# Performance work log

Hardware: AMD Instinct MI355X
Metric: run time of the kernel (lower is better)

The kernel has to match this reference:

```python
import jax, jax.numpy as jnp
import numpy as np

L, H, D, T, DFF, OUT, B = 6, 12, 49, 16, 1024, 10, 8192
STD = 0.02


def setup_inputs() -> dict:
    key = jax.random.key(0)
    ks = jax.random.split(key, 24)
    n = lambda k, shape: jax.random.normal(k, shape, dtype=jnp.float32) * STD
    return {
        "x": jax.random.normal(ks[0], (B, 784), dtype=jnp.float32),
        "mask": jnp.ones((B, T), dtype=bool),  # unused by the original Attention
        # per-layer, per-head Q/K/V/out linears (weights stored as (in, out))
        "Wq": n(ks[1], (L, H, D, D)), "bq": n(ks[2], (L, H, D)),
        "Wk": n(ks[3], (L, H, D, D)), "bk": n(ks[4], (L, H, D)),
        "Wv": n(ks[5], (L, H, D, D)), "bv": n(ks[6], (L, H, D)),
        "Wo": n(ks[7], (L, H, D, D)), "bo": n(ks[8], (L, H, D)),
        # concat projection Linear(D*H, D)
        "Wcat": n(ks[9], (L, H * D, D)), "bcat": n(ks[10], (L, D)),
        # LayerNorms
        "ln1_g": jnp.ones((L, D), jnp.float32), "ln1_b": jnp.zeros((L, D), jnp.float32),
        "ln2_g": jnp.ones((L, D), jnp.float32), "ln2_b": jnp.zeros((L, D), jnp.float32),
        # FeedForward
        "W1": n(ks[11], (L, D, DFF)), "b1": n(ks[12], (L, DFF)),
        "W2": n(ks[13], (L, DFF, D)), "b2": n(ks[14], (L, D)),
        # ClassificationHead
        "Wc": n(ks[15], (D, OUT)), "bc": n(ks[16], (OUT,)),
    }


def _ln(x, g, b):
    mu = jnp.mean(x, axis=-1, keepdims=True)
    var = jnp.mean((x - mu) ** 2, axis=-1, keepdims=True)
    return (x - mu) / jnp.sqrt(var + 1e-5) * g + b


def _forward(x, Wq, bq, Wk, bk, Wv, bv, Wo, bo, Wcat, bcat,
             ln1_g, ln1_b, ln2_g, ln2_b, W1, b1, W2, b2, Wc, bc):
    bsz = x.shape[0]
    h = x.reshape(bsz, T, D)  # MakeTokens
    scale = float(1.0 / np.sqrt(D))
    for i in range(L):
        xn = _ln(h, ln1_g[i], ln1_b[i])
        # all heads batched via einsum (each head attends over full d_model)
        q = jnp.einsum('btd,hde->bhte', xn, Wq[i]) + bq[i][None, :, None, :]
        k = jnp.einsum('btd,hde->bhte', xn, Wk[i]) + bk[i][None, :, None, :]
        v = jnp.einsum('btd,hde->bhte', xn, Wv[i]) + bv[i][None, :, None, :]
        w = jax.nn.softmax(jnp.einsum('bhte,bhse->bhts', q, k) * scale, axis=-1)
        o = jnp.einsum('bhts,bhse->bhte', w, v)
        o = jnp.einsum('bhte,hef->bhtf', o, Wo[i]) + bo[i][None, :, None, :]
        cat = o.transpose(0, 2, 1, 3).reshape(bsz, T, H * D)  # concat heads
        attn = cat @ Wcat[i] + bcat[i]
        x2 = h + attn  # dropout is identity at inference
        xn2 = _ln(x2, ln2_g[i], ln2_b[i])
        ff = jax.nn.relu(xn2 @ W1[i] + b1[i]) @ W2[i] + b2[i]
        h = x2 + ff
    return h[:, 0, :] @ Wc + bc  # ClassificationHead on token 0


def reference(x, mask, Wq, bq, Wk, bk, Wv, bv, Wo, bo, Wcat, bcat,
              ln1_g, ln1_b, ln2_g, ln2_b, W1, b1, W2, b2, Wc, bc):
    # mask is accepted but unused, matching the original Attention.forward
    return _forward(x, Wq, bq, Wk, bk, Wv, bv, Wo, bo, Wcat, bcat,
                    ln1_g, ln1_b, ln2_g, ln2_b, W1, b1, W2, b2, Wc, bc)
```

## Files before the change

kernel.cpp:

```cpp
#include <hip/hip_runtime.h>
#include <hip/hip_bf16.h>

#define LYR 6
#define NH 12
#define DM 49
#define FFD 1024
#define NOUT 10
#define NB 8192
#define NWIN 168
#define SPW 2

typedef __bf16 bf16x8 __attribute__((ext_vector_type(8)));
typedef float f32x4 __attribute__((ext_vector_type(4)));
typedef unsigned int u32;
typedef u32 u32x4 __attribute__((ext_vector_type(4)));

static __device__ __forceinline__ f32x4 mfma_full(u32x4 a, u32x4 b, f32x4 c) {
  return __builtin_amdgcn_mfma_f32_16x16x32_bf16(
      __builtin_bit_cast(bf16x8, a), __builtin_bit_cast(bf16x8, b), c, 0, 0, 0);
}

static __device__ __forceinline__ f32x4 mfma_hz(u32 a0, u32 a1, u32 b0, u32 b1, f32x4 c) {
  u32x4 A = {a0, a1, 0u, 0u};
  u32x4 B = {b0, b1, 0u, 0u};
  return mfma_full(A, B, c);
}

static __device__ __forceinline__ unsigned short f2bf(float f) {
  union { float f; unsigned u; } c; c.f = f;
  unsigned r = c.u + 0x7fffu + ((c.u >> 16) & 1u);
  return (unsigned short)(r >> 16);
}

static __device__ __forceinline__ u32 pk2(float a, float b) {
  __hip_bfloat162 h2 = __float22bfloat162_rn(make_float2(a, b));
  u32 r;
  __builtin_memcpy(&r, &h2, 4);
  return r;
}

static __device__ __forceinline__ void gload16(const void* gp, void* lp) {
  __builtin_amdgcn_global_load_lds(
      (const __attribute__((address_space(1))) unsigned int*)gp,
      (__attribute__((address_space(3))) unsigned int*)lp, 16, 0, 0);
}

static __device__ __forceinline__ void decode(int idx, int& d, int& col) {
  int tile = idx >> 10, ks = (idx >> 9) & 1, lane = (idx >> 3) & 63, j = idx & 7;
  col = 16 * tile + (lane & 15);
  d = 16 * (2 * ks + (j >= 4 ? 1 : 0)) + 4 * (lane >> 4) + (j & 3);
}


__global__ void prep_g_frag(const float* __restrict__ Wq, const float* __restrict__ bq,
                            const float* __restrict__ Wk, const float* __restrict__ bk,
                            unsigned short* __restrict__ blob) {
  const float QS = 1.44269504088896f / 7.0f;
  int lh = blockIdx.x, l = lh / NH, hd = lh % NH;
  unsigned short* base =
      blob + (size_t)(l * 28 + 2 * (hd >> 1)) * 8192 + (hd & 1) * 4096;
  for (int idx = threadIdx.x; idx < 4096; idx += blockDim.x) {
    int kk, cc;
    decode(idx, kk, cc);
    float acc = 0.f;
    if (cc <= DM && kk <= DM) {
      for (int e = 0; e < DM; ++e) {
        float kv = (cc < DM) ? Wk[(size_t)lh * 2401 + cc * DM + e] : bk[lh * DM + e];
        float qv = (kk < DM) ? Wq[(size_t)lh * 2401 + kk * DM + e] : bq[lh * DM + e];
        acc += kv * qv;
      }
      acc *= QS;
    }
    base[idx] = f2bf(acc);
  }
}

__global__ void prep_comb_f32(const float* __restrict__ Wo, const float* __restrict__ bo,
                              const float* __restrict__ Wcat, const float* __restrict__ bcat,
                              float* __restrict__ C) {
  int lh = blockIdx.x, l = lh / NH, hh = lh % NH;
  float* base = C + (size_t)lh * 3200;
  for (int idx = threadIdx.x; idx < 3200; idx += blockDim.x) {
    int e = idx >> 6, f = idx & 63;
    float val = 0.f;
    if (f < DM) {
      if (e < DM) {
        for (int c = 0; c < DM; ++c)
          val += Wo[(size_t)lh * 2401 + e * DM + c] *
                 Wcat[((size_t)l * 588 + hh * DM + c) * DM + f];
      } else {
        for (int c = 0; c < DM; ++c)
          val += bo[lh * DM + c] * Wcat[((size_t)l * 588 + hh * DM + c) * DM + f];
        if (hh == 0) val += bcat[l * DM + f];
      }
    }
    base[idx] = val;
  }
}

__global__ void prep_vc_frag(const float* __restrict__ Wv, const float* __restrict__ bv,
                             const float* __restrict__ C,
                             unsigned short* __restrict__ blob) {
  int lh = blockIdx.x, l = lh / NH, hd = lh % NH;
  const float* Cb = C + (size_t)lh * 3200;
  unsigned short* base =
      blob + (size_t)(l * 28 + 2 * (hd >> 1) + 1) * 8192 + (hd & 1) * 4096;
  for (int idx = threadIdx.x; idx < 4096; idx += blockDim.x) {
    int d, f;
    decode(idx, d, f);
    float acc = 0.f;
    if (f < DM && d <= DM) {
      for (int e = 0; e < DM; ++e) {
        float wv = (d < DM) ? Wv[(size_t)lh * 2401 + d * DM + e] : bv[lh * DM + e];
        acc += wv * Cb[e * 64 + f];
      }
      if (d == DM) acc += Cb[DM * 64 + f];
    }
    base[idx] = f2bf(acc);
  }
}

__global__ void prep_ff_frag(const float* __restrict__ W1, const float* __restrict__ b1,
                             const float* __restrict__ W2,
                             unsigned short* __restrict__ blob) {
  int l = blockIdx.x >> 3, part = blockIdx.x & 7;
  for (int idx = part * 16384 + threadIdx.x; idx < (part + 1) * 16384; idx += blockDim.x) {
    int c = idx >> 13, within = idx & 8191, sec = within >> 12, sidx = within & 4095;
    unsigned short* dst =
        blob + (size_t)(l * 28 + 12 + c) * 8192 + sec * 4096;
    int d, col;
    decode(sidx, d, col);
    float v = 0.f;
    if (sec == 0) {
      int jcol = 64 * c + col;
      if (d < DM) v = W1[(size_t)l * DM * FFD + d * FFD + jcol];
      else if (d == DM) v = b1[l * FFD + jcol];
    } else {
      int jg = 64 * c + d;
      if (col < DM) v = W2[(size_t)l * FFD * DM + jg * DM + col];
    }
    dst[sidx] = f2bf(v);
  }
}

__global__ void prep_small(const float* __restrict__ g1, const float* __restrict__ b1,
                           const float* __restrict__ g2, const float* __restrict__ b2,
                           const float* __restrict__ bff2,
                           float* __restrict__ g1p, float* __restrict__ b1p,
                           float* __restrict__ g2p, float* __restrict__ b2p,
                           float* __restrict__ bff2p) {
  int idx = threadIdx.x;
  if (idx >= 384) return;
  int l = idx >> 6, d = idx & 63;
  bool v = d < DM;
  g1p[idx] = v ? g1[l * DM + d] : 0.f;
  b1p[idx] = v ? b1[l * DM + d] : 0.f;
  g2p[idx] = v ? g2[l * DM + d] : 0.f;
  b2p[idx] = v ? b2[l * DM + d] : 0.f;
  bff2p[idx] = v ? bff2[l * DM + d] : 0.f;
}


static __device__ __forceinline__ void ln_pack(const f32x4 (&h)[4], const f32x4 (&gv)[4],
                                               const f32x4 (&bv)[4], int g, u32x4 (&xf)[2]) {
  float s = 0.f, s2 = 0.f;
#pragma unroll
  for (int mi = 0; mi < 4; ++mi)
#pragma unroll
    for (int r = 0; r < 4; ++r) { float v = h[mi][r]; s += v; s2 += v * v; }
  s += __shfl_xor(s, 16, 64); s += __shfl_xor(s, 32, 64);
  s2 += __shfl_xor(s2, 16, 64); s2 += __shfl_xor(s2, 32, 64);
  float mu = s * (1.f / 49.f);
  float rs = rsqrtf(s2 * (1.f / 49.f) - mu * mu + 1e-5f);
  u32 t[8];
#pragma unroll
  for (int mi = 0; mi < 4; ++mi) {
    float xv[4];
#pragma unroll
    for (int r = 0; r < 4; ++r) xv[r] = (h[mi][r] - mu) * rs * gv[mi][r] + bv[mi][r];
    if (mi == 3) xv[1] = (g == 0) ? 1.0f : xv[1];
    t[2 * mi] = pk2(xv[0], xv[1]);
    t[2 * mi + 1] = pk2(xv[2], xv[3]);
  }
  xf[0] = u32x4{t[0], t[1], t[2], t[3]};
  xf[1] = u32x4{t[4], t[5], t[6], t[7]};
}

static __device__ __forceinline__ void softmax_pk(f32x4 s, u32& p0, u32& p1) {
  float e0 = exp2f(s[0]), e1 = exp2f(s[1]);
  float e2 = exp2f(s[2]), e3 = exp2f(s[3]);
  float su = e0 + e1 + e2 + e3;
  su += __shfl_xor(su, 16, 64);
  su += __shfl_xor(su, 32, 64);
  float inv = 1.f / su;
  p0 = pk2(e0 * inv, e1 * inv);
  p1 = pk2(e2 * inv, e3 * inv);
}

#define STAGE_LOAD(s)                                                         \
  do {                                                                        \
    const unsigned short* gsrc = blob + (size_t)(s) * 8192 + tid * 8;         \
    unsigned short* ldst = &wbuf[(s) & 1][wv * 512];                          \
    _Pragma("unroll") for (int r = 0; r < 4; ++r)                             \
        gload16(gsrc + r * 2048, ldst + r * 2048);                            \
  } while (0)

__global__ __launch_bounds__(256, 4) void transformer_kernel(
    const float* __restrict__ x, float* __restrict__ out,
    const unsigned short* __restrict__ blob,
    const float* __restrict__ lg1, const float* __restrict__ lb1,
    const float* __restrict__ lg2, const float* __restrict__ lb2,
    const float* __restrict__ b2p, const float* __restrict__ Wc,
    const float* __restrict__ bc) {
  __shared__ __align__(16) unsigned short wbuf[2][8192];
  const int tid = threadIdx.x;
  const int wv = tid >> 6, lane = tid & 63;
  const int g = lane >> 4, li = lane & 15;
  const int s0 = blockIdx.x * 8 + wv * 2;
  const f32x4 z4 = {0.f, 0.f, 0.f, 0.f};

  STAGE_LOAD(0);

  f32x4 h[SPW][4];
#pragma unroll
  for (int s = 0; s < SPW; ++s) {
    const float* xa = x + (size_t)(s0 + s) * 784 + li * DM;
#pragma unroll
    for (int mi = 0; mi < 4; ++mi)
#pragma unroll
      for (int r = 0; r < 4; ++r) {
        int d = 16 * mi + 4 * g + r;
        h[s][mi][r] = (d < DM) ? xa[d] : 0.f;
      }
  }

  int w = 0;
  for (int layer = 0; layer < LYR; ++layer) {
    u32x4 xf[SPW][2];
    {
      f32x4 gv[4], bv[4];
#pragma unroll
      for (int mi = 0; mi < 4; ++mi) {
        int off = layer * 64 + 16 * mi + 4 * g;
        gv[mi] = *(const f32x4*)(lg1 + off);
        bv[mi] = *(const f32x4*)(lb1 + off);
      }
#pragma unroll
      for (int s = 0; s < SPW; ++s) ln_pack(h[s], gv, bv, g, xf[s]);
    }

    for (int hp = 0; hp < 6; ++hp) {
      __syncthreads();
      if (w + 1 < NWIN) STAGE_LOAD(w + 1);
      f32x4 sc[2][SPW];
#pragma unroll
      for (int hh = 0; hh < 2; ++hh) {
        const u32x4* GW = (const u32x4*)(wbuf[w & 1] + hh * 4096);
        __builtin_amdgcn_s_setprio(1);
        u32x4 yf[SPW][2];
#pragma unroll
        for (int mi = 0; mi < 4; ++mi) {
          f32x4 cy[SPW];
#pragma unroll
          for (int s = 0; s < SPW; ++s) cy[s] = z4;
#pragma unroll
          for (int ks = 0; ks < 2; ++ks) {
            u32x4 gw = GW[(mi * 2 + ks) * 64 + lane];
#pragma unroll
            for (int s = 0; s < SPW; ++s) cy[s] = mfma_full(gw, xf[s][ks], cy[s]);
          }
#pragma unroll
          for (int s = 0; s < SPW; ++s) {
            yf[s][mi >> 1][2 * (mi & 1)] = pk2(cy[s][0], cy[s][1]);
            yf[s][mi >> 1][2 * (mi & 1) + 1] = pk2(cy[s][2], cy[s][3]);
          }
        }
#pragma unroll
        for (int s = 0; s < SPW; ++s) {
          sc[hh][s] = mfma_full(xf[s][0], yf[s][0], z4);
          sc[hh][s] = mfma_full(xf[s][1], yf[s][1], sc[hh][s]);
        }
        __builtin_amdgcn_s_setprio(0);
      }
      ++w;

      __syncthreads();
      if (w + 1 < NWIN) STAGE_LOAD(w + 1);
#pragma unroll
      for (int hh = 0; hh < 2; ++hh) {
        const u32x4* UW = (const u32x4*)(wbuf[w & 1] + hh * 4096);
        __builtin_amdgcn_s_setprio(1);
        u32 uf[4][SPW][2];
#pragma unroll
        for (int nt = 0; nt < 4; ++nt) {
          f32x4 cu[SPW];
#pragma unroll
          for (int s = 0; s < SPW; ++s) cu[s] = z4;
#pragma unroll
          for (int ks = 0; ks < 2; ++ks) {
            u32x4 wu = UW[(nt * 2 + ks) * 64 + lane];
#pragma unroll
            for (int s = 0; s < SPW; ++s) cu[s] = mfma_full(xf[s][ks], wu, cu[s]);
          }
#pragma unroll
          for (int s = 0; s < SPW; ++s) {
            uf[nt][s][0] = pk2(cu[s][0], cu[s][1]);
            uf[nt][s][1] = pk2(cu[s][2], cu[s][3]);
          }
        }
        u32 p[SPW][2];
#pragma unroll
        for (int s = 0; s < SPW; ++s) softmax_pk(sc[hh][s], p[s][0], p[s][1]);
#pragma unroll
        for (int nt = 0; nt < 4; ++nt)
#pragma unroll
          for (int s = 0; s < SPW; ++s)
            h[s][nt] = mfma_hz(uf[nt][s][0], uf[nt][s][1], p[s][0], p[s][1], h[s][nt]);
        __builtin_amdgcn_s_setprio(0);
      }
      ++w;
    }

    {
      f32x4 gv[4], bv[4];
#pragma unroll
      for (int mi = 0; mi < 4; ++mi) {
        int off = layer * 64 + 16 * mi + 4 * g;
        gv[mi] = *(const f32x4*)(lg2 + off);
        bv[mi] = *(const f32x4*)(lb2 + off);
      }
#pragma unroll
      for (int s = 0; s < SPW; ++s) ln_pack(h[s], gv, bv, g, xf[s]);
#pragma unroll
      for (int mi = 0; mi < 4; ++mi) {
        f32x4 bb = *(const f32x4*)(b2p + layer * 64 + 16 * mi + 4 * g);
#pragma unroll
        for (int s = 0; s < SPW; ++s) h[s][mi] += bb;
      }
    }

    for (int c = 0; c < 16; ++c) {
      __syncthreads();
      if (w + 1 < NWIN) STAGE_LOAD(w + 1);
      const u32x4* W1c = (const u32x4*)wbuf[w & 1];
      const u32x4* W2c = (const u32x4*)(wbuf[w & 1] + 4096);
      __builtin_amdgcn_s_setprio(1);
      u32x4 af[SPW][2];
#pragma unroll
      for (int jt = 0; jt < 4; ++jt) {
        f32x4 ca[SPW];
#pragma unroll
        for (int s = 0; s < SPW; ++s) ca[s] = z4;
#pragma unroll
        for (int ks = 0; ks < 2; ++ks) {
          u32x4 ww = W1c[(jt * 2 + ks) * 64 + lane];
#pragma unroll
          for (int s = 0; s < SPW; ++s) ca[s] = mfma_full(ww, xf[s][ks], ca[s]);
        }
#pragma unroll
        for (int s = 0; s < SPW; ++s) {
          float r0 = fmaxf(ca[s][0], 0.f), r1 = fmaxf(ca[s][1], 0.f);
          float r2 = fmaxf(ca[s][2], 0.f), r3 = fmaxf(ca[s][3], 0.f);
          af[s][jt >> 1][2 * (jt & 1)] = pk2(r0, r1);
          af[s][jt >> 1][2 * (jt & 1) + 1] = pk2(r2, r3);
        }
      }
#pragma unroll
      for (int ft = 0; ft < 4; ++ft) {
#pragma unroll
        for (int ks = 0; ks < 2; ++ks) {
          u32x4 ww = W2c[(ft * 2 + ks) * 64 + lane];
#pragma unroll
          for (int s = 0; s < SPW; ++s) h[s][ft] = mfma_full(ww, af[s][ks], h[s][ft]);
        }
      }
      __builtin_amdgcn_s_setprio(0);
      ++w;
    }
  }

  __syncthreads();
  float* hs = (float*)&wbuf[0][0];
  if (li == 0) {
#pragma unroll
    for (int s = 0; s < SPW; ++s)
#pragma unroll
      for (int mi = 0; mi < 4; ++mi)
#pragma unroll
        for (int r = 0; r < 4; ++r)
          hs[(wv * SPW + s) * 64 + 16 * mi + 4 * g + r] = h[s][mi][r];
  }
  __syncthreads();
  if (lane < 10 * SPW) {
    int smp = lane / 10, c = lane % 10;
    float acc = bc[c];
    const float* hrow = hs + (wv * SPW + smp) * 64;
    for (int d = 0; d < DM; ++d) acc += hrow[d] * Wc[d * NOUT + c];
    out[(size_t)(s0 + smp) * NOUT + c] = acc;
  }
}

extern "C" void kernel_launch(void* const* d_in, const int* in_sizes, int n_in,
                              void* d_out, int out_size, void* d_ws, size_t ws_size,
                              hipStream_t stream) {
  const float* x = (const float*)d_in[0];
  const float* Wq = (const float*)d_in[2];
  const float* bq = (const float*)d_in[3];
  const float* Wk = (const float*)d_in[4];
  const float* bk = (const float*)d_in[5];
  const float* Wv = (const float*)d_in[6];
  const float* bv = (const float*)d_in[7];
  const float* Wo = (const float*)d_in[8];
  const float* bo = (const float*)d_in[9];
  const float* Wcat = (const float*)d_in[10];
  const float* bcat = (const float*)d_in[11];
  const float* ln1_g = (const float*)d_in[12];
  const float* ln1_b = (const float*)d_in[13];
  const float* ln2_g = (const float*)d_in[14];
  const float* ln2_b = (const float*)d_in[15];
  const float* W1 = (const float*)d_in[16];
  const float* b1 = (const float*)d_in[17];
  const float* W2 = (const float*)d_in[18];
  const float* b2 = (const float*)d_in[19];
  const float* Wc = (const float*)d_in[20];
  const float* bc = (const float*)d_in[21];

  unsigned short* blob = (unsigned short*)d_ws;
  float* Cscr = (float*)(blob + (size_t)NWIN * 8192);
  float* fp = Cscr + (size_t)72 * 3200;
  float* g1p = fp;
  float* b1p = g1p + 384;
  float* g2p = b1p + 384;
  float* b2lp = g2p + 384;
  float* b2p = b2lp + 384;

  prep_g_frag<<<72, 256, 0, stream>>>(Wq, bq, Wk, bk, blob);
  prep_comb_f32<<<72, 256, 0, stream>>>(Wo, bo, Wcat, bcat, Cscr);
  prep_vc_frag<<<72, 256, 0, stream>>>(Wv, bv, Cscr, blob);
  prep_ff_frag<<<48, 256, 0, stream>>>(W1, b1, W2, blob);
  prep_small<<<1, 384, 0, stream>>>(ln1_g, ln1_b, ln2_g, ln2_b, b2, g1p, b1p, g2p, b2lp, b2p);

  transformer_kernel<<<NB / 8, 256, 0, stream>>>(
      x, (float*)d_out, blob, g1p, b1p, g2p, b2lp, b2p, Wc, bc);
}
```

Baseline: 526.3 us.

## Software-pipeline FFN chunks by pairing W2 of previous chunk with W1 of next

Restructures the FFN loop so each staged window holds W1 for chunk k and W2 for chunk k-1. The W2 MFMAs of the previous chunk can then run alongside the W1 MFMAs of the current one, shortening dependency chains within a window. The weight blob layout is shifted per layer (29 windows instead of 28) to fit the skewed schedule. This adds one extra window and one extra barrier per layer, and drops the bounds check on most stage loads.

```diff
diff --git a/kernel.cpp b/kernel.cpp
--- a/kernel.cpp
+++ b/kernel.cpp
@@ -7,7 +7,7 @@
 #define FFD 1024
 #define NOUT 10
 #define NB 8192
-#define NWIN 168
+#define NWIN 174
 #define SPW 2
 
 typedef __bf16 bf16x8 __attribute__((ext_vector_type(8)));
@@ -58,7 +58,7 @@
   const float QS = 1.44269504088896f / 7.0f;
   int lh = blockIdx.x, l = lh / NH, hd = lh % NH;
   unsigned short* base =
-      blob + (size_t)(l * 28 + 2 * (hd >> 1)) * 8192 + (hd & 1) * 4096;
+      blob + (size_t)(l * 29 + 2 * (hd >> 1)) * 8192 + (hd & 1) * 4096;
   for (int idx = threadIdx.x; idx < 4096; idx += blockDim.x) {
     int kk, cc;
     decode(idx, kk, cc);
@@ -104,7 +104,7 @@
   int lh = blockIdx.x, l = lh / NH, hd = lh % NH;
   const float* Cb = C + (size_t)lh * 3200;
   unsigned short* base =
-      blob + (size_t)(l * 28 + 2 * (hd >> 1) + 1) * 8192 + (hd & 1) * 4096;
+      blob + (size_t)(l * 29 + 2 * (hd >> 1) + 1) * 8192 + (hd & 1) * 4096;
   for (int idx = threadIdx.x; idx < 4096; idx += blockDim.x) {
     int d, f;
     decode(idx, d, f);
@@ -127,7 +127,7 @@
   for (int idx = part * 16384 + threadIdx.x; idx < (part + 1) * 16384; idx += blockDim.x) {
     int c = idx >> 13, within = idx & 8191, sec = within >> 12, sidx = within & 4095;
     unsigned short* dst =
-        blob + (size_t)(l * 28 + 12 + c) * 8192 + sec * 4096;
+        blob + (size_t)(l * 29 + 12 + c + sec) * 8192 + sec * 4096;
     int d, col;
     decode(sidx, d, col);
     float v = 0.f;
@@ -251,7 +251,7 @@
 
     for (int hp = 0; hp < 6; ++hp) {
       __syncthreads();
-      if (w + 1 < NWIN) STAGE_LOAD(w + 1);
+      STAGE_LOAD(w + 1);
       f32x4 sc[2][SPW];
 #pragma unroll
       for (int hh = 0; hh < 2; ++hh) {
@@ -285,7 +285,7 @@
       ++w;
 
       __syncthreads();
-      if (w + 1 < NWIN) STAGE_LOAD(w + 1);
+      STAGE_LOAD(w + 1);
 #pragma unroll
       for (int hh = 0; hh < 2; ++hh) {
         const u32x4* UW = (const u32x4*)(wbuf[w & 1] + hh * 4096);
@@ -339,13 +339,46 @@
       }
     }
 
-    for (int c = 0; c < 16; ++c) {
+    u32x4 af[SPW][2];
+    {
       __syncthreads();
-      if (w + 1 < NWIN) STAGE_LOAD(w + 1);
+      STAGE_LOAD(w + 1);
+      const u32x4* W1c = (const u32x4*)wbuf[w & 1];
+      __builtin_amdgcn_s_setprio(1);
+#pragma unroll
+      for (int jt = 0; jt < 4; ++jt) {
+        f32x4 ca[SPW];
+#pragma unroll
+        for (int s = 0; s < SPW; ++s) ca[s] = z4;
+#pragma unroll
+        for (int ks = 0; ks < 2; ++ks) {
+          u32x4 ww = W1c[(jt * 2 + ks) * 64 + lane];
+#pragma unroll
+          for (int s = 0; s < SPW; ++s) ca[s] = mfma_full(ww, xf[s][ks], ca[s]);
+        }
+#pragma unroll
+        for (int s = 0; s < SPW; ++s) {
+          af[s][jt >> 1][2 * (jt & 1)] = pk2(fmaxf(ca[s][0], 0.f), fmaxf(ca[s][1], 0.f));
+          af[s][jt >> 1][2 * (jt & 1) + 1] = pk2(fmaxf(ca[s][2], 0.f), fmaxf(ca[s][3], 0.f));
+        }
+      }
+      __builtin_amdgcn_s_setprio(0);
+      ++w;
+    }
+    for (int k = 1; k < 16; ++k) {
+      __syncthreads();
+      STAGE_LOAD(w + 1);
       const u32x4* W1c = (const u32x4*)wbuf[w & 1];
       const u32x4* W2c = (const u32x4*)(wbuf[w & 1] + 4096);
       __builtin_amdgcn_s_setprio(1);
-      u32x4 af[SPW][2];
+#pragma unroll
+      for (int ft = 0; ft < 4; ++ft)
+#pragma unroll
+        for (int ks = 0; ks < 2; ++ks) {
+          u32x4 ww = W2c[(ft * 2 + ks) * 64 + lane];
+#pragma unroll
+          for (int s = 0; s < SPW; ++s) h[s][ft] = mfma_full(ww, af[s][ks], h[s][ft]);
+        }
 #pragma unroll
       for (int jt = 0; jt < 4; ++jt) {
         f32x4 ca[SPW];
@@ -359,21 +392,26 @@
         }
 #pragma unroll
         for (int s = 0; s < SPW; ++s) {
-          float r0 = fmaxf(ca[s][0], 0.f), r1 = fmaxf(ca[s][1], 0.f);
-          float r2 = fmaxf(ca[s][2], 0.f), r3 = fmaxf(ca[s][3], 0.f);
-          af[s][jt >> 1][2 * (jt & 1)] = pk2(r0, r1);
-          af[s][jt >> 1][2 * (jt & 1) + 1] = pk2(r2, r3);
-        }
-      }
-#pragma unroll
-      for (int ft = 0; ft < 4; ++ft) {
+          af[s][jt >> 1][2 * (jt & 1)] = pk2(fmaxf(ca[s][0], 0.f), fmaxf(ca[s][1], 0.f));
+          af[s][jt >> 1][2 * (jt & 1) + 1] = pk2(fmaxf(ca[s][2], 0.f), fmaxf(ca[s][3], 0.f));
+        }
+      }
+      __builtin_amdgcn_s_setprio(0);
+      ++w;
+    }
+    {
+      __syncthreads();
+      if (w + 1 < NWIN) STAGE_LOAD(w + 1);
+      const u32x4* W2c = (const u32x4*)(wbuf[w & 1] + 4096);
+      __builtin_amdgcn_s_setprio(1);
+#pragma unroll
+      for (int ft = 0; ft < 4; ++ft)
 #pragma unroll
         for (int ks = 0; ks < 2; ++ks) {
           u32x4 ww = W2c[(ft * 2 + ks) * 64 + lane];
 #pragma unroll
           for (int s = 0; s < SPW; ++s) h[s][ft] = mfma_full(ww, af[s][ks], h[s][ft]);
         }
-      }
       __builtin_amdgcn_s_setprio(0);
       ++w;
     }
```

Result: no change. 525.8 us (-0.1%).
